# Kernel tuning notes

Hardware: AMD Instinct MI355X
Metric: run time of the kernel (lower is better)

## Reference

```python
import jax, jax.numpy as jnp
import numpy as np

NUM_EMBEDDINGS = 4096
EMBEDDING_DIM = 256
COMMITMENT_COST = 0.25


def setup_inputs() -> dict:
    key = jax.random.key(0)
    k1, k2 = jax.random.split(key)
    z = jax.random.normal(k1, (16, 4096, EMBEDDING_DIM), dtype=jnp.float32)
    # nn.Embedding init: uniform(-1/K, 1/K)
    emb_w = jax.random.uniform(
        k2, (NUM_EMBEDDINGS, EMBEDDING_DIM), dtype=jnp.float32,
        minval=-1.0 / NUM_EMBEDDINGS, maxval=1.0 / NUM_EMBEDDINGS)
    return {"z": z, "emb_w": emb_w}


def reference(z, emb_w):
    B = z.shape[0]
    D = emb_w.shape[1]
    flat_z = z.reshape(-1, D)  # [T, D]
    # squared L2 distances: ||z||^2 - 2 z.E^T + ||e||^2  -> [T, K]
    distances = (jnp.sum(flat_z ** 2, axis=1, keepdims=True)
                 - 2.0 * flat_z @ emb_w.T
                 + jnp.sum(emb_w ** 2, axis=1))
    encoding_indices = jnp.argmin(distances, axis=1)  # [T]
    quantized = emb_w[encoding_indices]  # [T, D]
    # straight-through estimator
    quantized = flat_z + jax.lax.stop_gradient(quantized - flat_z)
    loss = (jnp.mean((jax.lax.stop_gradient(quantized) - flat_z) ** 2)
            + COMMITMENT_COST * jnp.mean((quantized - jax.lax.stop_gradient(flat_z)) ** 2))
    return (quantized.reshape(z.shape),
            encoding_indices.reshape(B, -1),
            loss)
```

## Files before the change

kernel.cpp:

```cpp
#include <hip/hip_runtime.h>
#include <cfloat>
#include <climits>

#define T_TOKENS 65536
#define K_EMB 4096
#define D_DIM 256
#define QOFF ((size_t)T_TOKENS * D_DIM)
#define WINDOW 1.2e-4f
#define B0 0.03125f

using bf16x8 = __attribute__((ext_vector_type(8))) short;
using f32x16 = __attribute__((ext_vector_type(16))) float;

__device__ __forceinline__ float fmul_nc(float a, float b) {
    float c = a * b;
    asm volatile("" : "+v"(c));
    return c;
}

__device__ __forceinline__ double wave_sum_d(double v) {
#pragma unroll
    for (int o = 32; o >= 1; o >>= 1) v += __shfl_down(v, o, 64);
    return v;
}

__device__ __forceinline__ void glds16(const void* g, void* l) {
    __builtin_amdgcn_global_load_lds((const __attribute__((address_space(1))) void*)g,
                                     (__attribute__((address_space(3))) void*)l, 16, 0, 0);
}

__device__ __forceinline__ unsigned short f2bf(float f) {
    unsigned u = __float_as_uint(f);
    u += 0x7FFFu + ((u >> 16) & 1u);
    return (unsigned short)(u >> 16);
}

__global__ __launch_bounds__(256)
void emb_prep_kernel(const float* __restrict__ emb, float* __restrict__ c32,
                     unsigned short* __restrict__ ehi) {
    const int k = blockIdx.x;
    const float e = emb[(size_t)k * D_DIM + threadIdx.x];
    ehi[(size_t)k * D_DIM + threadIdx.x] = f2bf(e);
    const double v = (double)e;
    double s = wave_sum_d(v * v);
    __shared__ double wsm[4];
    const int lane = threadIdx.x & 63, w = threadIdx.x >> 6;
    if (lane == 0) wsm[w] = s;
    __syncthreads();
    if (threadIdx.x == 0) c32[k] = (float)(wsm[0] + wsm[1] + wsm[2] + wsm[3]);
}

__global__ __launch_bounds__(256)
void argmin_mfma_kernel(const float* __restrict__ z,
                        const unsigned short* __restrict__ ehi,
                        unsigned int* __restrict__ keyout)
{
    __shared__ short lds_e[2][32 * 256];

    const int tid = threadIdx.x;
    const int wv  = tid >> 6;
    const int l   = tid & 63;
    const int lr  = l & 31;
    const int h   = l >> 5;
    const int tokA = blockIdx.x * 256 + wv * 64 + lr;
    const int tokB = tokA + 32;
    const int kbase = blockIdx.y * 2048;

    bf16x8 zA[16], zB[16];
#pragma unroll
    for (int st = 0; st < 16; st++) {
        {
            const float* zp = z + (size_t)tokA * D_DIM + st * 16 + h * 8;
            const float4 f0 = *(const float4*)zp;
            const float4 f1 = *(const float4*)(zp + 4);
            const float f[8] = {f0.x, f0.y, f0.z, f0.w, f1.x, f1.y, f1.z, f1.w};
#pragma unroll
            for (int j = 0; j < 8; j++) zA[st][j] = (short)f2bf(f[j]);
        }
        {
            const float* zp = z + (size_t)tokB * D_DIM + st * 16 + h * 8;
            const float4 f0 = *(const float4*)zp;
            const float4 f1 = *(const float4*)(zp + 4);
            const float f[8] = {f0.x, f0.y, f0.z, f0.w, f1.x, f1.y, f1.z, f1.w};
#pragma unroll
            for (int j = 0; j < 8; j++) zB[st][j] = (short)f2bf(f[j]);
        }
    }

    unsigned a1 = 0u, a2 = 0u, a3 = 0u, a4 = 0u;
    unsigned c1 = 0u, c2 = 0u, c3 = 0u, c4 = 0u;

    auto stage = [&](int buf, int ct) {
#pragma unroll
        for (int q = 0; q < 4; q++) {
            const int rp = wv * 4 + q;
            const int r  = 2 * rp + h;
            const int g  = lr ^ ((2 * q) | h);
            const unsigned short* src =
                ehi + (size_t)(kbase + ct * 32 + r) * D_DIM + g * 8;
            glds16(src, &lds_e[buf][rp * 512]);
        }
    };

    stage(0, 0);
    __syncthreads();

    const int lk = lr & 7;
    const short* lrow0 = &lds_e[0][lr * 256];
    const short* lrow1 = &lds_e[1][lr * 256];
    const unsigned vh4 = (unsigned)(4 * h);

    int buf = 0;
    for (int ct = 0; ct < 64; ct++) {
        if (ct + 1 < 64) stage(buf ^ 1, ct + 1);

        f32x16 pA, pB;
#pragma unroll
        for (int i = 0; i < 16; i++) { pA[i] = B0; pB[i] = B0; }

        const short* lrow = buf ? lrow1 : lrow0;
#pragma unroll
        for (int st = 0; st < 16; st++) {
            const bf16x8 eh = *(const bf16x8*)(lrow + (((2 * st + h) ^ lk) << 3));
            pA = __builtin_amdgcn_mfma_f32_32x32x16_bf16(eh, zA[st], pA, 0, 0, 0);
            pB = __builtin_amdgcn_mfma_f32_32x32x16_bf16(eh, zB[st], pB, 0, 0, 0);
        }

        const unsigned korb = (unsigned)(kbase + ct * 32) | vh4;
#pragma unroll
        for (int r = 0; r < 16; r++) {
            const unsigned rid = korb | (unsigned)((r & 3) + 8 * (r >> 2));
            unsigned t = (__float_as_uint(pA[r]) & 0xFFFFF000u) | rid;
            {
                const unsigned n1 = a1 > t ? a1 : t; t = a1 > t ? t : a1; a1 = n1;
                const unsigned n2 = a2 > t ? a2 : t; t = a2 > t ? t : a2; a2 = n2;
                const unsigned n3 = a3 > t ? a3 : t; t = a3 > t ? t : a3; a3 = n3;
                a4 = a4 > t ? a4 : t;
            }
            unsigned u = (__float_as_uint(pB[r]) & 0xFFFFF000u) | rid;
            {
                const unsigned n1 = c1 > u ? c1 : u; u = c1 > u ? u : c1; c1 = n1;
                const unsigned n2 = c2 > u ? c2 : u; u = c2 > u ? u : c2; c2 = n2;
                const unsigned n3 = c3 > u ? c3 : u; u = c3 > u ? u : c3; c3 = n3;
                c4 = c4 > u ? c4 : u;
            }
        }
        __syncthreads();
        buf ^= 1;
    }

    *(uint4*)(keyout + (((size_t)blockIdx.y * T_TOKENS + tokA) << 3) + vh4) =
        make_uint4(a1, a2, a3, a4);
    *(uint4*)(keyout + (((size_t)blockIdx.y * T_TOKENS + tokB) << 3) + vh4) =
        make_uint4(c1, c2, c3, c4);
}

__global__ __launch_bounds__(256)
void rescore_gather_kernel(const float* __restrict__ z, const float* __restrict__ emb,
                           const float* __restrict__ c32,
                           const unsigned int* __restrict__ keyout,
                           float* __restrict__ out, double* __restrict__ partials)
{
    __shared__ float zt[64][257];
    __shared__ float a32sm[64];
    __shared__ unsigned lmax[4][64];
    __shared__ float bvq[4][64];
    __shared__ int bkq[4][64];
    __shared__ int win[64];
    __shared__ double lsm[4];
    const int tid = threadIdx.x;
    const int base = blockIdx.x * 64;

    for (int idx = tid; idx < 64 * 256; idx += 256) {
        const int r = idx >> 8, c = idx & 255;
        zt[r][c] = z[(size_t)(base + r) * D_DIM + c];
    }
    __syncthreads();

    if (tid < 64) {
        const float* row = zt[tid];
        float S[2];
        for (int hh = 0; hh < 2; hh++) {
            const float* p = row + hh * 128;
            float r[8];
#pragma unroll
            for (int j = 0; j < 8; j++) r[j] = fmul_nc(p[j], p[j]);
            for (int m = 1; m < 16; m++) {
#pragma unroll
                for (int j = 0; j < 8; j++) r[j] += fmul_nc(p[8 * m + j], p[8 * m + j]);
            }
            S[hh] = ((r[0] + r[1]) + (r[2] + r[3])) + ((r[4] + r[5]) + (r[6] + r[7]));
        }
        a32sm[tid] = S[0] + S[1];
    }

    const int ti = tid & 63, qq = tid >> 6;
    const int t = base + ti;
    const uint4 kk = *(const uint4*)(keyout +
        (((size_t)(qq >> 1) * T_TOKENS + t) << 3) + (qq & 1) * 4);
    unsigned lm = kk.x > kk.y ? kk.x : kk.y;
    lm = lm > kk.z ? lm : kk.z;
    lm = lm > kk.w ? lm : kk.w;
    lmax[qq][ti] = lm;
    __syncthreads();

    unsigned gm = lmax[0][ti];
#pragma unroll
    for (int e = 1; e < 4; e++) gm = gm > lmax[e][ti] ? gm : lmax[e][ti];
    const float thr = __uint_as_float(gm) - WINDOW;
    const float ar = a32sm[ti];
    float bestv = FLT_MAX; int bestk = INT_MAX;
    const unsigned ks[4] = {kk.x, kk.y, kk.z, kk.w};
#pragma unroll
    for (int s = 0; s < 4; s++) {
        if (__uint_as_float(ks[s]) >= thr) {
            const int k = (int)(ks[s] & 0xFFFu);
            const float* er = emb + (size_t)k * D_DIM;
            float m = 0.0f;
#pragma unroll 8
            for (int d4 = 0; d4 < 64; d4++) {
                const float4 e4 = *(const float4*)(er + 4 * d4);
                m = fmaf(zt[ti][4 * d4 + 0], e4.x, m);
                m = fmaf(zt[ti][4 * d4 + 1], e4.y, m);
                m = fmaf(zt[ti][4 * d4 + 2], e4.z, m);
                m = fmaf(zt[ti][4 * d4 + 3], e4.w, m);
            }
            const float v1 = ar - 2.0f * m;
            const float v2 = v1 + c32[k];
            if (v2 < bestv || (v2 == bestv && k < bestk)) { bestv = v2; bestk = k; }
        }
    }
    bvq[qq][ti] = bestv; bkq[qq][ti] = bestk;
    __syncthreads();

    if (tid < 64) {
        float B = bvq[0][tid];
        int I = bkq[0][tid];
#pragma unroll
        for (int e = 1; e < 4; e++) {
            const float cv = bvq[e][tid];
            const int ck = bkq[e][tid];
            if (cv < B || (cv == B && ck < I)) { B = cv; I = ck; }
        }
        win[tid] = I;
    }
    __syncthreads();

    double lacc = 0.0;
    for (int ti2 = 0; ti2 < 64; ti2++) {
        const int sel = win[ti2];
        const float ev = emb[(size_t)sel * D_DIM + tid];
        const float zv = zt[ti2][tid];
        out[(size_t)(base + ti2) * D_DIM + tid] = ev;
        if (tid == 0) out[QOFF + base + ti2] = (float)sel;
        const double df = (double)zv - (double)ev;
        lacc += df * df;
    }
    lacc = wave_sum_d(lacc);
    const int lane = tid & 63, w = tid >> 6;
    if (lane == 0) lsm[w] = lacc;
    __syncthreads();
    if (tid == 0) partials[blockIdx.x] = lsm[0] + lsm[1] + lsm[2] + lsm[3];
}

__global__ void finalize_kernel(const double* __restrict__ partials, float* __restrict__ out) {
    __shared__ double rsm[4];
    const int tid = threadIdx.x;
    double s = 0.0;
    for (int i = tid; i < 1024; i += 256) s += partials[i];
    s = wave_sum_d(s);
    if ((tid & 63) == 0) rsm[tid >> 6] = s;
    __syncthreads();
    if (tid == 0) {
        const double mean = (rsm[0] + rsm[1] + rsm[2] + rsm[3]) / (double)QOFF;
        out[QOFF + T_TOKENS] = (float)(1.25 * mean);
    }
}

extern "C" void kernel_launch(void* const* d_in, const int* in_sizes, int n_in,
                              void* d_out, int out_size, void* d_ws, size_t ws_size,
                              hipStream_t stream)
{
    const float* z = (const float*)d_in[0];
    const float* emb = (const float*)d_in[1];
    float* out = (float*)d_out;
    char* ws = (char*)d_ws;

    float* c32 = (float*)ws;
    unsigned int* keyout = (unsigned int*)(ws + 16384);
    unsigned short* ehi = (unsigned short*)(ws + 4210688);
    double* partials = (double*)(ws + 6307840);

    emb_prep_kernel<<<K_EMB, 256, 0, stream>>>(emb, c32, ehi);
    argmin_mfma_kernel<<<dim3(T_TOKENS / 256, 2), 256, 0, stream>>>(z, ehi, keyout);
    rescore_gather_kernel<<<T_TOKENS / 64, 256, 0, stream>>>(z, emb, c32, keyout, out, partials);
    finalize_kernel<<<1, 256, 0, stream>>>(partials, out);
}
```

Measured before the change: 372.4 us.

## Split codebook across four K-chunks and vectorize gather/loss epilogue

The argmin MFMA kernel's grid now covers four codebook chunks of 1024 entries instead of two of 2048. That doubles the number of blocks (1024 total) for better CU occupancy, and each block runs half as many tiles. The rescore kernel now reads 8 candidate keys per chunk from 4 chunks, one per wave, and rescores up to 8 candidates per thread. The workspace layout grows to hold the larger keyout buffer. The gather/loss epilogue now gives each wave 16 tokens with float4 loads and stores instead of scalar per-thread loops. The trade-off is that the z-tile load and bf16 conversion are repeated twice as often, plus more keyout traffic.

```diff
diff --git a/kernel.cpp b/kernel.cpp
--- a/kernel.cpp
+++ b/kernel.cpp
@@ -8,6 +8,9 @@
 #define QOFF ((size_t)T_TOKENS * D_DIM)
 #define WINDOW 1.2e-4f
 #define B0 0.03125f
+#define KSPLIT 4
+#define KCHUNK (K_EMB / KSPLIT)
+#define NTILES (KCHUNK / 32)
 
 using bf16x8 = __attribute__((ext_vector_type(8))) short;
 using f32x16 = __attribute__((ext_vector_type(16))) float;
@@ -64,7 +67,7 @@
     const int h   = l >> 5;
     const int tokA = blockIdx.x * 256 + wv * 64 + lr;
     const int tokB = tokA + 32;
-    const int kbase = blockIdx.y * 2048;
+    const int kbase = blockIdx.y * KCHUNK;
 
     bf16x8 zA[16], zB[16];
 #pragma unroll
@@ -111,8 +114,8 @@
     const unsigned vh4 = (unsigned)(4 * h);
 
     int buf = 0;
-    for (int ct = 0; ct < 64; ct++) {
-        if (ct + 1 < 64) stage(buf ^ 1, ct + 1);
+    for (int ct = 0; ct < NTILES; ct++) {
+        if (ct + 1 < NTILES) stage(buf ^ 1, ct + 1);
 
         f32x16 pA, pB;
 #pragma unroll
@@ -196,11 +199,12 @@
 
     const int ti = tid & 63, qq = tid >> 6;
     const int t = base + ti;
-    const uint4 kk = *(const uint4*)(keyout +
-        (((size_t)(qq >> 1) * T_TOKENS + t) << 3) + (qq & 1) * 4);
-    unsigned lm = kk.x > kk.y ? kk.x : kk.y;
-    lm = lm > kk.z ? lm : kk.z;
-    lm = lm > kk.w ? lm : kk.w;
+    const uint4 k0 = *(const uint4*)(keyout + (((size_t)qq * T_TOKENS + t) << 3));
+    const uint4 k1 = *(const uint4*)(keyout + (((size_t)qq * T_TOKENS + t) << 3) + 4);
+    const unsigned ks[8] = {k0.x, k0.y, k0.z, k0.w, k1.x, k1.y, k1.z, k1.w};
+    unsigned lm = 0u;
+#pragma unroll
+    for (int s = 0; s < 8; s++) lm = lm > ks[s] ? lm : ks[s];
     lmax[qq][ti] = lm;
     __syncthreads();
 
@@ -210,9 +214,8 @@
     const float thr = __uint_as_float(gm) - WINDOW;
     const float ar = a32sm[ti];
     float bestv = FLT_MAX; int bestk = INT_MAX;
-    const unsigned ks[4] = {kk.x, kk.y, kk.z, kk.w};
-#pragma unroll
-    for (int s = 0; s < 4; s++) {
+#pragma unroll
+    for (int s = 0; s < 8; s++) {
         if (__uint_as_float(ks[s]) >= thr) {
             const int k = (int)(ks[s] & 0xFFFu);
             const float* er = emb + (size_t)k * D_DIM;
@@ -246,18 +249,24 @@
     }
     __syncthreads();
 
+    const int lane = tid & 63, w = tid >> 6;
     double lacc = 0.0;
-    for (int ti2 = 0; ti2 < 64; ti2++) {
+#pragma unroll 4
+    for (int s = 0; s < 16; s++) {
+        const int ti2 = w * 16 + s;
         const int sel = win[ti2];
-        const float ev = emb[(size_t)sel * D_DIM + tid];
-        const float zv = zt[ti2][tid];
-        out[(size_t)(base + ti2) * D_DIM + tid] = ev;
-        if (tid == 0) out[QOFF + base + ti2] = (float)sel;
-        const double df = (double)zv - (double)ev;
-        lacc += df * df;
+        const float4 e4 = *(const float4*)(emb + (size_t)sel * D_DIM + 4 * lane);
+        const float z0 = zt[ti2][4 * lane + 0], z1 = zt[ti2][4 * lane + 1];
+        const float z2 = zt[ti2][4 * lane + 2], z3 = zt[ti2][4 * lane + 3];
+        *(float4*)(out + (size_t)(base + ti2) * D_DIM + 4 * lane) = e4;
+        if (lane == 0) out[QOFF + base + ti2] = (float)sel;
+        const double d0 = (double)z0 - (double)e4.x;
+        const double d1 = (double)z1 - (double)e4.y;
+        const double d2 = (double)z2 - (double)e4.z;
+        const double d3 = (double)z3 - (double)e4.w;
+        lacc += d0 * d0 + d1 * d1 + d2 * d2 + d3 * d3;
     }
     lacc = wave_sum_d(lacc);
-    const int lane = tid & 63, w = tid >> 6;
     if (lane == 0) lsm[w] = lacc;
     __syncthreads();
     if (tid == 0) partials[blockIdx.x] = lsm[0] + lsm[1] + lsm[2] + lsm[3];
@@ -288,11 +297,11 @@
 
     float* c32 = (float*)ws;
     unsigned int* keyout = (unsigned int*)(ws + 16384);
-    unsigned short* ehi = (unsigned short*)(ws + 4210688);
-    double* partials = (double*)(ws + 6307840);
+    unsigned short* ehi = (unsigned short*)(ws + 8404992);
+    double* partials = (double*)(ws + 10502144);
 
     emb_prep_kernel<<<K_EMB, 256, 0, stream>>>(emb, c32, ehi);
-    argmin_mfma_kernel<<<dim3(T_TOKENS / 256, 2), 256, 0, stream>>>(z, ehi, keyout);
+    argmin_mfma_kernel<<<dim3(T_TOKENS / 256, KSPLIT), 256, 0, stream>>>(z, ehi, keyout);
     rescore_gather_kernel<<<T_TOKENS / 64, 256, 0, stream>>>(z, emb, c32, keyout, out, partials);
     finalize_kernel<<<1, 256, 0, stream>>>(partials, out);
 }
```

Result: no change. 377.6 us (+1.4%).
